# Optimization experiments

Measured on AMD Instinct MI355X. Metric: run time of the kernel, lower is better.

## Reference

```python
import jax, jax.numpy as jnp
import numpy as np

N_NODES = 100000
N_EDGES = 640000
D_IN = 128
D_OUT = 128

def setup_inputs() -> dict:
    key = jax.random.key(0)
    k1, k2, k3, k4, k5 = jax.random.split(key, 5)
    feat = jax.random.normal(k1, (N_NODES, D_IN), dtype=jnp.float32)
    src = jax.random.randint(k2, (N_EDGES,), 0, N_NODES, dtype=jnp.int32)
    dst = jax.random.randint(k3, (N_EDGES,), 0, N_NODES, dtype=jnp.int32)
    scale = 1.0 / np.sqrt(D_IN)
    W_self = jax.random.normal(k4, (D_IN, D_OUT), dtype=jnp.float32) * scale
    W_neigh = jax.random.normal(k5, (D_IN, D_OUT), dtype=jnp.float32) * scale
    b_self = jnp.zeros((D_OUT,), dtype=jnp.float32)
    b_neigh = jnp.zeros((D_OUT,), dtype=jnp.float32)
    return {"feat": feat, "src": src, "dst": dst,
            "W_self": W_self, "b_self": b_self,
            "W_neigh": W_neigh, "b_neigh": b_neigh}

def reference(feat, src, dst, W_self, b_self, W_neigh, b_neigh):
    # GraphSAGE 'mean' aggregator: copy_src + mean reduce over in-edges, then
    # rst = fc_self(h_self) + fc_neigh(h_neigh). feat_drop=0, no activation/norm.
    n = feat.shape[0]
    msg = feat[src]                                   # [E, D_in] gather
    neigh_sum = jax.ops.segment_sum(msg, dst, num_segments=n)      # [N, D_in]
    deg = jax.ops.segment_sum(jnp.ones_like(dst, dtype=feat.dtype), dst,
                              num_segments=n)          # [N]
    # mean with zero-in-degree nodes -> 0 (DGL semantics)
    h_neigh = neigh_sum / jnp.maximum(deg, 1.0)[:, None]
    rst = feat @ W_self + b_self + h_neigh @ W_neigh + b_neigh      # [N, D_out]
    return rst
```

## Files before the change

kernel.cpp:

```cpp
#include <hip/hip_runtime.h>


constexpr int N_NODES = 100000;
constexpr int N_EDGES = 640000;
constexpr int D = 128;

constexpr int SCAN_ELEMS_PER_BLOCK = 1024;
constexpr int SCAN_NBLOCKS = (N_NODES + SCAN_ELEMS_PER_BLOCK - 1) / SCAN_ELEMS_PER_BLOCK;

typedef __attribute__((ext_vector_type(8))) short bf16x8;
typedef __attribute__((ext_vector_type(4))) float f32x4;
typedef __attribute__((ext_vector_type(2))) float f32x2;

__device__ __forceinline__ unsigned short f2bf(float f) {
    unsigned int u = __float_as_uint(f);
    unsigned int r = u + 0x7FFFu + ((u >> 16) & 1u);
    return (unsigned short)(r >> 16);
}


__global__ void deg_kernel(const int* __restrict__ dst, int* __restrict__ deg) {
    int e = blockIdx.x * blockDim.x + threadIdx.x;
    if (e < N_EDGES) atomicAdd(&deg[dst[e]], 1);
}

__global__ __launch_bounds__(256) void partial_kernel(const int* __restrict__ deg,
                                                      int* __restrict__ bsum) {
    __shared__ int wsum[4];
    const int tid = threadIdx.x;
    const int base = (blockIdx.x * 256 + tid) * 4;
    int s = 0;
    #pragma unroll
    for (int j = 0; j < 4; j++) {
        int idx = base + j;
        if (idx < N_NODES) s += deg[idx];
    }
    for (int off = 32; off > 0; off >>= 1) s += __shfl_down(s, off, 64);
    if ((tid & 63) == 0) wsum[tid >> 6] = s;
    __syncthreads();
    if (tid == 0) bsum[blockIdx.x] = wsum[0] + wsum[1] + wsum[2] + wsum[3];
}

__global__ __launch_bounds__(128) void scanb_kernel(const int* __restrict__ bsum,
                                                    int* __restrict__ boff,
                                                    int* __restrict__ rowptr) {
    __shared__ int s[128];
    const int tid = threadIdx.x;
    int v = (tid < SCAN_NBLOCKS) ? bsum[tid] : 0;
    s[tid] = v;
    __syncthreads();
    for (int off = 1; off < 128; off <<= 1) {
        int u = (tid >= off) ? s[tid - off] : 0;
        __syncthreads();
        s[tid] += u;
        __syncthreads();
    }
    if (tid < SCAN_NBLOCKS) boff[tid] = s[tid] - v;
    if (tid == 0) rowptr[N_NODES] = N_EDGES;
}

__global__ __launch_bounds__(256) void final_kernel(const int* __restrict__ deg,
                                                    const int* __restrict__ boff,
                                                    int* __restrict__ rowptr,
                                                    int* __restrict__ cursor) {
    __shared__ int wsum[4];
    const int tid = threadIdx.x;
    const int lane = tid & 63;
    const int wave = tid >> 6;
    const int base = (blockIdx.x * 256 + tid) * 4;

    int local[4];
    int tsum = 0;
    #pragma unroll
    for (int j = 0; j < 4; j++) {
        int idx = base + j;
        local[j] = (idx < N_NODES) ? deg[idx] : 0;
        tsum += local[j];
    }
    int incl = tsum;
    for (int off = 1; off < 64; off <<= 1) {
        int u = __shfl_up(incl, off, 64);
        if (lane >= off) incl += u;
    }
    if (lane == 63) wsum[wave] = incl;
    __syncthreads();
    int woff = 0;
    for (int w = 0; w < 4; w++) woff += (w < wave) ? wsum[w] : 0;

    int run = boff[blockIdx.x] + woff + (incl - tsum);
    #pragma unroll
    for (int j = 0; j < 4; j++) {
        int idx = base + j;
        if (idx < N_NODES) {
            rowptr[idx] = run;
            cursor[idx] = run;
            run += local[j];
        }
    }
}

__global__ void fill_kernel(const int* __restrict__ src, const int* __restrict__ dst,
                            int* __restrict__ cursor, int* __restrict__ csr_src) {
    int e = blockIdx.x * blockDim.x + threadIdx.x;
    if (e < N_EDGES) {
        int pos = atomicAdd(&cursor[dst[e]], 1);
        csr_src[pos] = src[e];
    }
}

__global__ void wprep_kernel(const float* __restrict__ Ws, const float* __restrict__ Wn,
                             unsigned short* __restrict__ wp) {
    int i = blockIdx.x * 256 + threadIdx.x;
    if (i >= 2 * D * D) return;
    int r  = i & 7;
    int c  = (i >> 3) & 127;
    int h  = (i >> 10) & 3;
    int ks = (i >> 12) & 3;
    int m  = i >> 14;
    const float* W = m ? Wn : Ws;
    int k = ks * 32 + h * 8 + r;
    wp[i] = f2bf(W[k * D + c]);
}

__global__ __launch_bounds__(256) void mmfused_kernel(
    const float* __restrict__ feat, const unsigned short* __restrict__ wp,
    const float* __restrict__ b_self, const float* __restrict__ b_neigh,
    float* __restrict__ out, unsigned short* __restrict__ t)
{
    __shared__ unsigned short lw[2 * 4 * 4 * 128 * 8];

    const int tid = threadIdx.x;
    {
        const uint4* s = (const uint4*)wp;
        uint4* d = (uint4*)lw;
        #pragma unroll
        for (int i = 0; i < 16; i++) d[tid + i * 256] = s[tid + i * 256];
    }
    __syncthreads();

    const int wave = tid >> 6, lane = tid & 63;
    const int h = lane >> 4, c = lane & 15;
    const int row_base = blockIdx.x * 256 + wave * 64;

    bf16x8 a[4][4];
    #pragma unroll
    for (int ti = 0; ti < 4; ti++) {
        int row = row_base + ti * 16 + c;
        int rowc = min(row, N_NODES - 1);
        const float4* fr = (const float4*)(feat + (size_t)rowc * D);
        #pragma unroll
        for (int ks = 0; ks < 4; ks++) {
            float4 u = fr[ks * 8 + h * 2];
            float4 v = fr[ks * 8 + h * 2 + 1];
            bf16x8 f;
            f[0] = (short)f2bf(u.x); f[1] = (short)f2bf(u.y);
            f[2] = (short)f2bf(u.z); f[3] = (short)f2bf(u.w);
            f[4] = (short)f2bf(v.x); f[5] = (short)f2bf(v.y);
            f[6] = (short)f2bf(v.z); f[7] = (short)f2bf(v.w);
            a[ti][ks] = f;
        }
    }

    #pragma unroll
    for (int m = 0; m < 2; m++) {
        for (int ct = 0; ct < 8; ct++) {
            bf16x8 b[4];
            #pragma unroll
            for (int ks = 0; ks < 4; ks++)
                b[ks] = ((const bf16x8*)lw)[((m * 4 + ks) * 4 + h) * 128 + ct * 16 + c];

            f32x4 acc[4];
            #pragma unroll
            for (int ti = 0; ti < 4; ti++) acc[ti] = f32x4{0.f, 0.f, 0.f, 0.f};
            #pragma unroll
            for (int ks = 0; ks < 4; ks++)
                #pragma unroll
                for (int ti = 0; ti < 4; ti++)
                    acc[ti] = __builtin_amdgcn_mfma_f32_16x16x32_bf16(a[ti][ks], b[ks], acc[ti], 0, 0, 0);

            const int col = ct * 16 + c;
            if (m == 0) {
                const float bias = b_self[col] + b_neigh[col];
                #pragma unroll
                for (int ti = 0; ti < 4; ti++) {
                    if (row_base + ti * 16 < N_NODES) {
                        #pragma unroll
                        for (int q = 0; q < 4; q++) {
                            int row = row_base + ti * 16 + h * 4 + q;
                            out[(size_t)row * D + col] = acc[ti][q] + bias;
                        }
                    }
                }
            } else {
                #pragma unroll
                for (int ti = 0; ti < 4; ti++) {
                    if (row_base + ti * 16 < N_NODES) {
                        #pragma unroll
                        for (int q = 0; q < 4; q++) {
                            int row = row_base + ti * 16 + h * 4 + q;
                            t[(size_t)row * D + col] = f2bf(acc[ti][q]);
                        }
                    }
                }
            }
        }
    }
}

__global__ __launch_bounds__(256) void gather_kernel(
    const unsigned short* __restrict__ t, const int* __restrict__ csr_src,
    const int* __restrict__ rowptr, float* __restrict__ out)
{
    const int lane = threadIdx.x & 63;
    const int wid = (blockIdx.x * blockDim.x + threadIdx.x) >> 6;
    const int nw = (gridDim.x * blockDim.x) >> 6;

    for (int n = wid; n < N_NODES; n += nw) {
        const int e0 = rowptr[n];
        const int e1 = rowptr[n + 1];
        float ax = 0.f, ay = 0.f;
        int e = e0;
        for (; e + 4 <= e1; e += 4) {
            const int s0 = csr_src[e], s1 = csr_src[e + 1];
            const int s2 = csr_src[e + 2], s3 = csr_src[e + 3];
            const unsigned int v0 = ((const unsigned int*)(t + (size_t)s0 * D))[lane];
            const unsigned int v1 = ((const unsigned int*)(t + (size_t)s1 * D))[lane];
            const unsigned int v2 = ((const unsigned int*)(t + (size_t)s2 * D))[lane];
            const unsigned int v3 = ((const unsigned int*)(t + (size_t)s3 * D))[lane];
            ax += __uint_as_float(v0 << 16) + __uint_as_float(v1 << 16)
                + __uint_as_float(v2 << 16) + __uint_as_float(v3 << 16);
            ay += __uint_as_float(v0 & 0xFFFF0000u) + __uint_as_float(v1 & 0xFFFF0000u)
                + __uint_as_float(v2 & 0xFFFF0000u) + __uint_as_float(v3 & 0xFFFF0000u);
        }
        for (; e < e1; e++) {
            const int s = csr_src[e];
            const unsigned int v = ((const unsigned int*)(t + (size_t)s * D))[lane];
            ax += __uint_as_float(v << 16);
            ay += __uint_as_float(v & 0xFFFF0000u);
        }
        const float sc = 1.0f / (float)max(e1 - e0, 1);
        f32x2* orow = (f32x2*)(out + (size_t)n * D) + lane;
        f32x2 o = __builtin_nontemporal_load(orow);
        o.x += ax * sc;
        o.y += ay * sc;
        __builtin_nontemporal_store(o, orow);
    }
}

extern "C" void kernel_launch(void* const* d_in, const int* in_sizes, int n_in,
                              void* d_out, int out_size, void* d_ws, size_t ws_size,
                              hipStream_t stream) {
    const float* feat    = (const float*)d_in[0];
    const int*   src     = (const int*)d_in[1];
    const int*   dst     = (const int*)d_in[2];
    const float* W_self  = (const float*)d_in[3];
    const float* b_self  = (const float*)d_in[4];
    const float* W_neigh = (const float*)d_in[5];
    const float* b_neigh = (const float*)d_in[6];
    float* out = (float*)d_out;

    unsigned short* t  = (unsigned short*)d_ws;
    unsigned short* wp = t + (size_t)N_NODES * D;
    int*   deg     = (int*)(wp + 2 * D * D);
    int*   rowptr  = deg + N_NODES;
    int*   cursor  = rowptr + (N_NODES + 1);
    int*   csr_src = cursor + N_NODES;
    int*   bsum    = csr_src + N_EDGES;
    int*   boff    = bsum + SCAN_NBLOCKS;

    (void)hipMemsetAsync(deg, 0, N_NODES * sizeof(int), stream);
    deg_kernel<<<(N_EDGES + 255) / 256, 256, 0, stream>>>(dst, deg);

    partial_kernel<<<SCAN_NBLOCKS, 256, 0, stream>>>(deg, bsum);
    scanb_kernel<<<1, 128, 0, stream>>>(bsum, boff, rowptr);
    final_kernel<<<SCAN_NBLOCKS, 256, 0, stream>>>(deg, boff, rowptr, cursor);

    fill_kernel<<<(N_EDGES + 255) / 256, 256, 0, stream>>>(src, dst, cursor, csr_src);

    wprep_kernel<<<(2 * D * D + 255) / 256, 256, 0, stream>>>(W_self, W_neigh, wp);

    mmfused_kernel<<<(N_NODES + 255) / 256, 256, 0, stream>>>(feat, wp, b_self, b_neigh, out, t);

    gather_kernel<<<25000, 256, 0, stream>>>(t, csr_src, rowptr, out);
}
```

Before: 152.6 us.

## Fuse weight prep into degree kernel, shrink GEMM tile, batch gather index loads

Weight bf16 packing moves into the degree-count kernel, which removes one launch. The fused GEMM now handles 128 rows per block instead of 256, giving more blocks and fewer registers per wave at the cost of reloading the LDS weights more often. The gather kernel assigns exactly one wave per node. It loads up to 16 CSR indices per wave in a single coalesced load and broadcasts them with readlane, so 16 independent row loads can be in flight, replacing the serial scalar index loads.

```diff
diff --git a/kernel.cpp b/kernel.cpp
--- a/kernel.cpp
+++ b/kernel.cpp
@@ -19,9 +19,22 @@
 }
 
 
-__global__ void deg_kernel(const int* __restrict__ dst, int* __restrict__ deg) {
+__global__ void deg_wprep_kernel(const int* __restrict__ dst, int* __restrict__ deg,
+                                 const float* __restrict__ Ws, const float* __restrict__ Wn,
+                                 unsigned short* __restrict__ wp) {
     int e = blockIdx.x * blockDim.x + threadIdx.x;
     if (e < N_EDGES) atomicAdd(&deg[dst[e]], 1);
+    if (e < 2 * D * D) {
+        int i = e;
+        int r  = i & 7;
+        int c  = (i >> 3) & 127;
+        int h  = (i >> 10) & 3;
+        int ks = (i >> 12) & 3;
+        int m  = i >> 14;
+        const float* W = m ? Wn : Ws;
+        int k = ks * 32 + h * 8 + r;
+        wp[i] = f2bf(W[k * D + c]);
+    }
 }
 
 __global__ __launch_bounds__(256) void partial_kernel(const int* __restrict__ deg,
@@ -108,20 +121,6 @@
     }
 }
 
-__global__ void wprep_kernel(const float* __restrict__ Ws, const float* __restrict__ Wn,
-                             unsigned short* __restrict__ wp) {
-    int i = blockIdx.x * 256 + threadIdx.x;
-    if (i >= 2 * D * D) return;
-    int r  = i & 7;
-    int c  = (i >> 3) & 127;
-    int h  = (i >> 10) & 3;
-    int ks = (i >> 12) & 3;
-    int m  = i >> 14;
-    const float* W = m ? Wn : Ws;
-    int k = ks * 32 + h * 8 + r;
-    wp[i] = f2bf(W[k * D + c]);
-}
-
 __global__ __launch_bounds__(256) void mmfused_kernel(
     const float* __restrict__ feat, const unsigned short* __restrict__ wp,
     const float* __restrict__ b_self, const float* __restrict__ b_neigh,
@@ -140,11 +139,11 @@
 
     const int wave = tid >> 6, lane = tid & 63;
     const int h = lane >> 4, c = lane & 15;
-    const int row_base = blockIdx.x * 256 + wave * 64;
-
-    bf16x8 a[4][4];
-    #pragma unroll
-    for (int ti = 0; ti < 4; ti++) {
+    const int row_base = blockIdx.x * 128 + wave * 32;
+
+    bf16x8 a[2][4];
+    #pragma unroll
+    for (int ti = 0; ti < 2; ti++) {
         int row = row_base + ti * 16 + c;
         int rowc = min(row, N_NODES - 1);
         const float4* fr = (const float4*)(feat + (size_t)rowc * D);
@@ -169,20 +168,20 @@
             for (int ks = 0; ks < 4; ks++)
                 b[ks] = ((const bf16x8*)lw)[((m * 4 + ks) * 4 + h) * 128 + ct * 16 + c];
 
-            f32x4 acc[4];
+            f32x4 acc[2];
             #pragma unroll
-            for (int ti = 0; ti < 4; ti++) acc[ti] = f32x4{0.f, 0.f, 0.f, 0.f};
+            for (int ti = 0; ti < 2; ti++) acc[ti] = f32x4{0.f, 0.f, 0.f, 0.f};
             #pragma unroll
             for (int ks = 0; ks < 4; ks++)
                 #pragma unroll
-                for (int ti = 0; ti < 4; ti++)
+                for (int ti = 0; ti < 2; ti++)
                     acc[ti] = __builtin_amdgcn_mfma_f32_16x16x32_bf16(a[ti][ks], b[ks], acc[ti], 0, 0, 0);
 
             const int col = ct * 16 + c;
             if (m == 0) {
                 const float bias = b_self[col] + b_neigh[col];
                 #pragma unroll
-                for (int ti = 0; ti < 4; ti++) {
+                for (int ti = 0; ti < 2; ti++) {
                     if (row_base + ti * 16 < N_NODES) {
                         #pragma unroll
                         for (int q = 0; q < 4; q++) {
@@ -193,7 +192,7 @@
                 }
             } else {
                 #pragma unroll
-                for (int ti = 0; ti < 4; ti++) {
+                for (int ti = 0; ti < 2; ti++) {
                     if (row_base + ti * 16 < N_NODES) {
                         #pragma unroll
                         for (int q = 0; q < 4; q++) {
@@ -212,39 +211,39 @@
     const int* __restrict__ rowptr, float* __restrict__ out)
 {
     const int lane = threadIdx.x & 63;
-    const int wid = (blockIdx.x * blockDim.x + threadIdx.x) >> 6;
-    const int nw = (gridDim.x * blockDim.x) >> 6;
-
-    for (int n = wid; n < N_NODES; n += nw) {
-        const int e0 = rowptr[n];
-        const int e1 = rowptr[n + 1];
-        float ax = 0.f, ay = 0.f;
-        int e = e0;
-        for (; e + 4 <= e1; e += 4) {
-            const int s0 = csr_src[e], s1 = csr_src[e + 1];
-            const int s2 = csr_src[e + 2], s3 = csr_src[e + 3];
-            const unsigned int v0 = ((const unsigned int*)(t + (size_t)s0 * D))[lane];
-            const unsigned int v1 = ((const unsigned int*)(t + (size_t)s1 * D))[lane];
-            const unsigned int v2 = ((const unsigned int*)(t + (size_t)s2 * D))[lane];
-            const unsigned int v3 = ((const unsigned int*)(t + (size_t)s3 * D))[lane];
-            ax += __uint_as_float(v0 << 16) + __uint_as_float(v1 << 16)
-                + __uint_as_float(v2 << 16) + __uint_as_float(v3 << 16);
-            ay += __uint_as_float(v0 & 0xFFFF0000u) + __uint_as_float(v1 & 0xFFFF0000u)
-                + __uint_as_float(v2 & 0xFFFF0000u) + __uint_as_float(v3 & 0xFFFF0000u);
-        }
-        for (; e < e1; e++) {
-            const int s = csr_src[e];
-            const unsigned int v = ((const unsigned int*)(t + (size_t)s * D))[lane];
-            ax += __uint_as_float(v << 16);
-            ay += __uint_as_float(v & 0xFFFF0000u);
-        }
-        const float sc = 1.0f / (float)max(e1 - e0, 1);
-        f32x2* orow = (f32x2*)(out + (size_t)n * D) + lane;
-        f32x2 o = __builtin_nontemporal_load(orow);
-        o.x += ax * sc;
-        o.y += ay * sc;
-        __builtin_nontemporal_store(o, orow);
-    }
+    const int n = (blockIdx.x * blockDim.x + threadIdx.x) >> 6;
+    if (n >= N_NODES) return;
+
+    const int e0 = rowptr[n];
+    const int e1 = rowptr[n + 1];
+
+    f32x2* orow = (f32x2*)(out + (size_t)n * D) + lane;
+    f32x2 o = __builtin_nontemporal_load(orow);
+
+    float ax = 0.f, ay = 0.f;
+    for (int base = e0; base < e1; base += 16) {
+        const int cnt = min(16, e1 - base);
+        int myidx = (lane < cnt) ? csr_src[base + lane] : 0;
+        unsigned int vv[16];
+        #pragma unroll
+        for (int j = 0; j < 16; j++) {
+            if (j < cnt) {
+                int s = __builtin_amdgcn_readlane(myidx, j);
+                vv[j] = ((const unsigned int*)(t + (size_t)s * D))[lane];
+            }
+        }
+        #pragma unroll
+        for (int j = 0; j < 16; j++) {
+            if (j < cnt) {
+                ax += __uint_as_float(vv[j] << 16);
+                ay += __uint_as_float(vv[j] & 0xFFFF0000u);
+            }
+        }
+    }
+    const float sc = 1.0f / (float)max(e1 - e0, 1);
+    o.x += ax * sc;
+    o.y += ay * sc;
+    __builtin_nontemporal_store(o, orow);
 }
 
 extern "C" void kernel_launch(void* const* d_in, const int* in_sizes, int n_in,
@@ -269,7 +268,7 @@
     int*   boff    = bsum + SCAN_NBLOCKS;
 
     (void)hipMemsetAsync(deg, 0, N_NODES * sizeof(int), stream);
-    deg_kernel<<<(N_EDGES + 255) / 256, 256, 0, stream>>>(dst, deg);
+    deg_wprep_kernel<<<(N_EDGES + 255) / 256, 256, 0, stream>>>(dst, deg, W_self, W_neigh, wp);
 
     partial_kernel<<<SCAN_NBLOCKS, 256, 0, stream>>>(deg, bsum);
     scanb_kernel<<<1, 128, 0, stream>>>(bsum, boff, rowptr);
@@ -277,9 +276,7 @@
 
     fill_kernel<<<(N_EDGES + 255) / 256, 256, 0, stream>>>(src, dst, cursor, csr_src);
 
-    wprep_kernel<<<(2 * D * D + 255) / 256, 256, 0, stream>>>(W_self, W_neigh, wp);
-
-    mmfused_kernel<<<(N_NODES + 255) / 256, 256, 0, stream>>>(feat, wp, b_self, b_neigh, out, t);
+    mmfused_kernel<<<(N_NODES + 127) / 128, 256, 0, stream>>>(feat, wp, b_self, b_neigh, out, t);
 
     gather_kernel<<<25000, 256, 0, stream>>>(t, csr_src, rowptr, out);
 }
```

Result: slower. 160.2 us (+5.0%).
